# Kernel optimization log

Hardware: AMD Instinct MI355X
Metric: run time of the kernel (lower is better)

The kernel has to match this reference:

```python
import jax, jax.numpy as jnp
import numpy as np

SIGMA2_MU = 0.5  # hyper_params['sigma2_mu']
R = 128          # number of spatial basis functions
NV = 2000        # number of query points
KM1 = 30         # K - 1


def setup_inputs() -> dict:
    key = jax.random.key(0)
    k1, k2, k3, k4 = jax.random.split(key, 4)
    Xi_evals = jax.random.normal(k1, (R, NV), dtype=jnp.float32)
    vec_W_post_mean = jax.random.normal(k2, (R * KM1, 1), dtype=jnp.float32)
    vec_W_post_cov = jax.random.normal(k3, (R * KM1, R * KM1), dtype=jnp.float32)
    C_mu = jax.random.normal(k4, (NV, 1), dtype=jnp.float32)
    return {"Xi_evals": Xi_evals, "vec_W_post_mean": vec_W_post_mean,
            "vec_W_post_cov": vec_W_post_cov, "C_mu": C_mu}


def reference(Xi_evals, vec_W_post_mean, vec_W_post_cov, C_mu):
    # Xi_evals: (r, Nv); vec_W_post_mean: (r*(K-1), 1); vec_W_post_cov: (r*(K-1), r*(K-1))
    r, Nv = Xi_evals.shape
    Km1 = vec_W_post_mean.shape[0] // r
    K = Km1 + 1
    X = Xi_evals.T                                # (Nv, r)
    # kron(x^T, I_{K-1}) @ w  ==  X @ W  with W = w.reshape(r, K-1)
    W = vec_W_post_mean.reshape(r, Km1)
    Post_mean_c = X @ W                           # (Nv, K-1)
    # kron(x^T, I) @ Cov @ kron(x, I): quadratic form over r-blocks
    C4 = vec_W_post_cov.reshape(r, Km1, r, Km1)   # (i, k, j, l)
    A = jnp.einsum('vi,ikjl->vkjl', X, C4)        # (Nv, K-1, r, K-1)
    Post_cov_c = jnp.einsum('vkjl,vj->vkl', A, X) # (Nv, K-1, K-1)
    Post_mean_coefs = jnp.concatenate([C_mu, Post_mean_c], axis=1)  # (Nv, K)
    Post_cov_mats = jnp.zeros((Nv, K, K), dtype=Xi_evals.dtype)
    Post_cov_mats = Post_cov_mats.at[:, 0, 0].set(SIGMA2_MU)
    Post_cov_mats = Post_cov_mats.at[:, 1:, 1:].set(Post_cov_c)
    return Post_mean_coefs, Post_cov_mats
```

## Files before the change

kernel.cpp:

```cpp
#include <hip/hip_runtime.h>

typedef _Float16 f16;
typedef _Float16 f16x8 __attribute__((ext_vector_type(8)));
typedef float    f32x16 __attribute__((ext_vector_type(16)));

#define NV      2000
#define RR      128
#define KM1     30
#define KKOUT   31
#define NQ      900
#define QQ      961
#define COV_OFF 62000

#define B5_BYTES 17104896
#define XH_BYTES 524288

#define PERM_BLKS  3840
#define XC1_BLKS   128
#define ZERO_BLKS  1877
#define MEAN_BLKS  248
#define PREP_GRID  (PERM_BLKS + XC1_BLKS + ZERO_BLKS + MEAN_BLKS)

__global__ void prep_kernel(const float* __restrict__ Xi,
                            const float* __restrict__ Wm,
                            const float* __restrict__ cov,
                            const float* __restrict__ Cmu,
                            f16* __restrict__ B5,
                            f16* __restrict__ Xh,
                            float* __restrict__ outm,
                            float* __restrict__ oc) {
    __shared__ float rowS[3840];
    int b = blockIdx.x, tid = threadIdx.x;
    if (b < PERM_BLKS) {
        int i = b / 30, k = b - i * 30;
        int g = i >> 4;
        int j0 = g << 4;
        int W = 128 - j0;
        int lo = (i - j0) * 30;
        const float* src = cov + (size_t)b * 3840 + j0 * 30;
        for (int t = tid; t < W * 30; t += 256)
            rowS[t] = (t >= lo) ? src[t] : 0.f;
        __syncthreads();
        int n2 = (127 - i) * 15;
        for (int idx = tid; idx < n2; idx += 256) {
            int j = i + 1 + idx / 15;
            int p = idx - (j - i - 1) * 15;
            const float2 v2 = *(const float2*)(cov + (size_t)(j * 30 + k) * 3840 + i * 30 + 2 * p);
            rowS[(j - j0) * 30 + 2 * p]     += v2.x;
            rowS[(j - j0) * 30 + 2 * p + 1] += v2.y;
        }
        __syncthreads();
        int t_st = i & 15;
        int nOct = W >> 3;
        for (int it = tid; it < nOct * 30; it += 256) {
            int oct = it / 30, l = it - oct * 30;
            int j = j0 + oct * 8;
            int s = j >> 4, kq = (j >> 3) & 1;
            int q = k * 30 + l, qt = q >> 5, l31 = q & 31;
            int kz, slot;
            if (g < 4) { kz = g;     slot = s - g; }
            else       { kz = 7 - g; slot = s + 1; }
            f16 vals[8];
#pragma unroll
            for (int d = 0; d < 8; ++d) vals[d] = (f16)rowS[(j + d - j0) * 30 + l];
            f16* dst = B5 + ((((size_t)(qt * 4 + kz) * 16 + t_st) * 9 + slot) << 9)
                          + (kq * 32 + l31) * 8;
            *(uint4*)dst = *(uint4*)vals;
        }
        return;
    }
    b -= PERM_BLKS;
    if (b < XC1_BLKS) {
        int t = b * 256 + tid;
        int v = t & 2047, rc = t >> 11;
        f16 vals[8];
#pragma unroll
        for (int d = 0; d < 8; ++d) {
            float x = (v < NV) ? Xi[(rc * 8 + d) * NV + v] : 0.f;
            vals[d] = (f16)x;
        }
        *(uint4*)(Xh + (size_t)v * 128 + rc * 8) = *(uint4*)vals;
        return;
    }
    b -= XC1_BLKS;
    if (b < ZERO_BLKS) {
        size_t idx = ((size_t)b * 256 + tid) * 4;
        if (idx < (size_t)NV * QQ) {
            unsigned rem = (unsigned)(idx % QQ);
            float4 zv;
            zv.x = (rem == 0u)   ? 0.5f : 0.f;
            zv.y = (rem == 960u) ? 0.5f : 0.f;
            zv.z = (rem == 959u) ? 0.5f : 0.f;
            zv.w = (rem == 958u) ? 0.5f : 0.f;
            *(float4*)(oc + idx) = zv;
        }
        return;
    }
    b -= ZERO_BLKS;
    int t2 = b * 256 + tid;
    int c = t2 >> 11, v = t2 & 2047;
    if (v >= NV || c >= KKOUT) return;
    if (c == 0) { outm[(size_t)v * KKOUT] = Cmu[v]; return; }
    float acc = 0.f;
    const float* w = Wm + (c - 1);
#pragma unroll 8
    for (int i = 0; i < RR; ++i)
        acc = fmaf(Xi[i * NV + v], w[i * KM1], acc);
    outm[(size_t)v * KKOUT + c] = acc;
}

__device__ __forceinline__ void gl2lds16(const f16* g, f16* l) {
    __builtin_amdgcn_global_load_lds(
        (const __attribute__((address_space(1))) unsigned int*)(const void*)g,
        (__attribute__((address_space(3))) unsigned int*)(void*)l,
        16, 0, 0);
}

template<int KZ>
__device__ __forceinline__ void gemm_body(const f16* __restrict__ B5,
                                          const f16* __restrict__ Xh,
                                          float* __restrict__ out_cov,
                                          int qt, int y, f16* lbuf) {
    constexpr int NA = 8 - KZ, NB = 1 + KZ, NS = 8 - KZ, UB = 7 - 2 * KZ;
    const int tid = threadIdx.x, lane = tid & 63, w = tid >> 6;
    const int l31 = lane & 31, kq = lane >> 5;
    const int v0 = y * 512 + w * 128;
    const int vr = v0 + l31;

    f16x8 xj[4][NS];
#pragma unroll
    for (int fm = 0; fm < 4; ++fm)
#pragma unroll
        for (int u = 0; u < NS; ++u)
            xj[fm][u] = *(const f16x8*)(Xh + (size_t)(vr + fm * 32) * 128 + (KZ + u) * 16 + kq * 8);

    const f16* gbase = B5 + ((size_t)(qt * 4 + KZ) * 16) * 4608 + lane * 8;

    f32x16 acc[4] = {};

#pragma unroll
    for (int r = 0; r < 3; ++r) {
        int m = w + 4 * r;
        if (m < 9) gl2lds16(gbase + m * 512, lbuf + m * 512);
    }
    __syncthreads();

#pragma unroll
    for (int t = 0; t < 16; ++t) {
        const int cur = t & 1;
        if (t < 15) {
            const f16* gs = gbase + (size_t)(t + 1) * 4608;
            f16* ls = lbuf + (cur ^ 1) * 4608;
#pragma unroll
            for (int r = 0; r < 3; ++r) {
                int m = w + 4 * r;
                if (m < 9) gl2lds16(gs + m * 512, ls + m * 512);
            }
        }
        const int srcl = l31 + ((t >> 3) << 5);
        f16x8 xsA[4], xsB[4];
#pragma unroll
        for (int fm = 0; fm < 4; ++fm) {
            unsigned short ha = __builtin_bit_cast(unsigned short, (f16)xj[fm][0][t & 7]);
            unsigned short hb = __builtin_bit_cast(unsigned short, (f16)xj[fm][UB][t & 7]);
            int pa = __shfl((int)ha, srcl, 64);
            int pb = __shfl((int)hb, srcl, 64);
            f16 xa = __builtin_bit_cast(f16, (unsigned short)pa);
            f16 xb = __builtin_bit_cast(f16, (unsigned short)pb);
#pragma unroll
            for (int d = 0; d < 8; ++d) { xsA[fm][d] = xa; xsB[fm][d] = xb; }
        }
        const f16* lb = lbuf + cur * 4608 + lane * 8;
#pragma unroll
        for (int m = 0; m < NA; ++m) {
            f16x8 bf = *(const f16x8*)(lb + m * 512);
#pragma unroll
            for (int fm = 0; fm < 4; ++fm)
                acc[fm] = __builtin_amdgcn_mfma_f32_32x32x16_f16(xsA[fm] * xj[fm][m], bf, acc[fm], 0, 0, 0);
        }
#pragma unroll
        for (int m2 = 0; m2 < NB; ++m2) {
            f16x8 bf = *(const f16x8*)(lb + (NA + m2) * 512);
#pragma unroll
            for (int fm = 0; fm < 4; ++fm)
                acc[fm] = __builtin_amdgcn_mfma_f32_32x32x16_f16(xsB[fm] * xj[fm][UB + m2], bf, acc[fm], 0, 0, 0);
        }
        __syncthreads();
    }

    const int q = qt * 32 + l31;
    if (q >= NQ) return;
    const int kk = q / 30, ll = q - kk * 30;
    float* cb = out_cov + (kk + 1) * KKOUT + (ll + 1);
#pragma unroll
    for (int fm = 0; fm < 4; ++fm) {
        int vb = v0 + fm * 32 + 4 * kq;
#pragma unroll
        for (int r = 0; r < 16; ++r) {
            int v = vb + (r & 3) + 8 * (r >> 2);
            if (v < NV) atomicAdd(cb + (size_t)v * QQ, acc[fm][r]);
        }
    }
}

__launch_bounds__(256, 2)
__global__ void gemm5_kernel(const f16* __restrict__ B5,
                             const f16* __restrict__ Xh,
                             float* __restrict__ out_cov) {
    __shared__ f16 lbuf[2 * 4608];
    const int bid = blockIdx.x;
    const int xcd = bid & 7, base = bid >> 3;
    const int y = base & 3, s3 = base >> 2;
    const int S = s3 * 8 + xcd;
    const int qt = S >> 2, kz = S & 3;
    if (qt >= 29) return;
    switch (kz) {
        case 0:  gemm_body<0>(B5, Xh, out_cov, qt, y, lbuf); break;
        case 1:  gemm_body<1>(B5, Xh, out_cov, qt, y, lbuf); break;
        case 2:  gemm_body<2>(B5, Xh, out_cov, qt, y, lbuf); break;
        default: gemm_body<3>(B5, Xh, out_cov, qt, y, lbuf); break;
    }
}

extern "C" void kernel_launch(void* const* d_in, const int* in_sizes, int n_in,
                              void* d_out, int out_size, void* d_ws, size_t ws_size,
                              hipStream_t stream) {
    const float* Xi  = (const float*)d_in[0];
    const float* Wm  = (const float*)d_in[1];
    const float* Cov = (const float*)d_in[2];
    const float* Cmu = (const float*)d_in[3];
    float* out      = (float*)d_out;
    float* out_mean = out;
    float* out_cov  = out + COV_OFF;
    f16* B5 = (f16*)d_ws;
    f16* Xh = (f16*)((char*)d_ws + B5_BYTES);

    prep_kernel <<<PREP_GRID, 256, 0, stream>>>(Xi, Wm, Cov, Cmu, B5, Xh,
                                                out_mean, out_cov);
    gemm5_kernel<<<480, 256, 0, stream>>>(B5, Xh, out_cov);
}
```

Baseline: 170.9 us.

## Load B fragments directly from global into registers instead of LDS double-buffer

Drops the LDS double-buffered async global-to-LDS staging of the B tiles. Each wave now loads all nine B fragments for a step straight from global memory into registers, which removes the per-step __syncthreads barriers. The broadcast X scalar multiply also becomes a scalar-times-vector product instead of building splat vectors. In exchange every wave fetches the same B data separately (four times the L2/global traffic per block), loses explicit prefetch overlap, and holds more registers per thread.

```diff
diff --git a/kernel.cpp b/kernel.cpp
--- a/kernel.cpp
+++ b/kernel.cpp
@@ -109,18 +109,11 @@
     outm[(size_t)v * KKOUT + c] = acc;
 }
 
-__device__ __forceinline__ void gl2lds16(const f16* g, f16* l) {
-    __builtin_amdgcn_global_load_lds(
-        (const __attribute__((address_space(1))) unsigned int*)(const void*)g,
-        (__attribute__((address_space(3))) unsigned int*)(void*)l,
-        16, 0, 0);
-}
-
 template<int KZ>
 __device__ __forceinline__ void gemm_body(const f16* __restrict__ B5,
                                           const f16* __restrict__ Xh,
                                           float* __restrict__ out_cov,
-                                          int qt, int y, f16* lbuf) {
+                                          int qt, int y) {
     constexpr int NA = 8 - KZ, NB = 1 + KZ, NS = 8 - KZ, UB = 7 - 2 * KZ;
     const int tid = threadIdx.x, lane = tid & 63, w = tid >> 6;
     const int l31 = lane & 31, kq = lane >> 5;
@@ -139,53 +132,35 @@
     f32x16 acc[4] = {};
 
 #pragma unroll
-    for (int r = 0; r < 3; ++r) {
-        int m = w + 4 * r;
-        if (m < 9) gl2lds16(gbase + m * 512, lbuf + m * 512);
-    }
-    __syncthreads();
-
-#pragma unroll
     for (int t = 0; t < 16; ++t) {
-        const int cur = t & 1;
-        if (t < 15) {
-            const f16* gs = gbase + (size_t)(t + 1) * 4608;
-            f16* ls = lbuf + (cur ^ 1) * 4608;
-#pragma unroll
-            for (int r = 0; r < 3; ++r) {
-                int m = w + 4 * r;
-                if (m < 9) gl2lds16(gs + m * 512, ls + m * 512);
-            }
-        }
+        f16x8 bfv[9];
+#pragma unroll
+        for (int m = 0; m < 9; ++m)
+            bfv[m] = *(const f16x8*)(gbase + (size_t)t * 4608 + m * 512);
+
         const int srcl = l31 + ((t >> 3) << 5);
-        f16x8 xsA[4], xsB[4];
+        f16 xA[4], xB[4];
 #pragma unroll
         for (int fm = 0; fm < 4; ++fm) {
             unsigned short ha = __builtin_bit_cast(unsigned short, (f16)xj[fm][0][t & 7]);
             unsigned short hb = __builtin_bit_cast(unsigned short, (f16)xj[fm][UB][t & 7]);
             int pa = __shfl((int)ha, srcl, 64);
             int pb = __shfl((int)hb, srcl, 64);
-            f16 xa = __builtin_bit_cast(f16, (unsigned short)pa);
-            f16 xb = __builtin_bit_cast(f16, (unsigned short)pb);
-#pragma unroll
-            for (int d = 0; d < 8; ++d) { xsA[fm][d] = xa; xsB[fm][d] = xb; }
-        }
-        const f16* lb = lbuf + cur * 4608 + lane * 8;
+            xA[fm] = __builtin_bit_cast(f16, (unsigned short)pa);
+            xB[fm] = __builtin_bit_cast(f16, (unsigned short)pb);
+        }
 #pragma unroll
         for (int m = 0; m < NA; ++m) {
-            f16x8 bf = *(const f16x8*)(lb + m * 512);
 #pragma unroll
             for (int fm = 0; fm < 4; ++fm)
-                acc[fm] = __builtin_amdgcn_mfma_f32_32x32x16_f16(xsA[fm] * xj[fm][m], bf, acc[fm], 0, 0, 0);
+                acc[fm] = __builtin_amdgcn_mfma_f32_32x32x16_f16(xj[fm][m] * xA[fm], bfv[m], acc[fm], 0, 0, 0);
         }
 #pragma unroll
         for (int m2 = 0; m2 < NB; ++m2) {
-            f16x8 bf = *(const f16x8*)(lb + (NA + m2) * 512);
 #pragma unroll
             for (int fm = 0; fm < 4; ++fm)
-                acc[fm] = __builtin_amdgcn_mfma_f32_32x32x16_f16(xsB[fm] * xj[fm][UB + m2], bf, acc[fm], 0, 0, 0);
-        }
-        __syncthreads();
+                acc[fm] = __builtin_amdgcn_mfma_f32_32x32x16_f16(xj[fm][UB + m2] * xB[fm], bfv[NA + m2], acc[fm], 0, 0, 0);
+        }
     }
 
     const int q = qt * 32 + l31;
@@ -207,7 +182,6 @@
 __global__ void gemm5_kernel(const f16* __restrict__ B5,
                              const f16* __restrict__ Xh,
                              float* __restrict__ out_cov) {
-    __shared__ f16 lbuf[2 * 4608];
     const int bid = blockIdx.x;
     const int xcd = bid & 7, base = bid >> 3;
     const int y = base & 3, s3 = base >> 2;
@@ -215,10 +189,10 @@
     const int qt = S >> 2, kz = S & 3;
     if (qt >= 29) return;
     switch (kz) {
-        case 0:  gemm_body<0>(B5, Xh, out_cov, qt, y, lbuf); break;
-        case 1:  gemm_body<1>(B5, Xh, out_cov, qt, y, lbuf); break;
-        case 2:  gemm_body<2>(B5, Xh, out_cov, qt, y, lbuf); break;
-        default: gemm_body<3>(B5, Xh, out_cov, qt, y, lbuf); break;
+        case 0:  gemm_body<0>(B5, Xh, out_cov, qt, y); break;
+        case 1:  gemm_body<1>(B5, Xh, out_cov, qt, y); break;
+        case 2:  gemm_body<2>(B5, Xh, out_cov, qt, y); break;
+        default: gemm_body<3>(B5, Xh, out_cov, qt, y); break;
     }
 }
 
```

After: 176.1 us. 3.0% more time.
